# Kernel optimization log

Hardware: AMD Instinct MI355X
Metric: run time of the kernel (lower is better)

Reference implementation:

```python
import jax, jax.numpy as jnp
import numpy as np

B, C, OUTC, H, W, K, P, S = 4, 64, 64, 128, 128, 3, 1, 1
KK = K * K


def setup_inputs() -> dict:
    key = jax.random.key(0)
    ks = jax.random.split(key, 5)
    x = jax.random.normal(ks[0], (B, C, H, W), dtype=jnp.float32)
    # small-scale offset weights keep learned offsets in a realistic few-pixel range
    w_off = jax.random.normal(ks[1], (2 * KK, C, 3, 3), dtype=jnp.float32) * 0.05
    b_off = jnp.zeros((2 * KK,), dtype=jnp.float32)
    w_mask = jax.random.normal(ks[2], (KK, C, 3, 3), dtype=jnp.float32) * 0.05
    b_mask = jnp.zeros((KK,), dtype=jnp.float32)
    w_dcn = jax.random.normal(ks[3], (OUTC, C, K, K), dtype=jnp.float32) * (1.0 / np.sqrt(C * KK))
    b_dcn = jnp.zeros((OUTC,), dtype=jnp.float32)
    return {"x": x, "w_off": w_off, "b_off": b_off, "w_mask": w_mask,
            "b_mask": b_mask, "w_dcn": w_dcn, "b_dcn": b_dcn}


def _conv3x3(x, w, b):
    y = jax.lax.conv_general_dilated(x, w, (1, 1), ((1, 1), (1, 1)),
                                     dimension_numbers=("NCHW", "OIHW", "NCHW"))
    return y + b[None, :, None, None]


def _deform_conv(x, offset, mask, w, b):
    # torchvision DeformConv2d (v2, modulated). offset layout: [B, kk, (dy,dx), H, W]
    Ho = (H + 2 * P - K) // S + 1
    Wo = (W + 2 * P - K) // S + 1
    off = offset.reshape(B, KK, 2, Ho, Wo)
    dy, dx = off[:, :, 0], off[:, :, 1]                      # [B,kk,Ho,Wo]
    ki, kj = jnp.meshgrid(jnp.arange(K), jnp.arange(K), indexing="ij")
    ki = ki.reshape(KK).astype(jnp.float32)
    kj = kj.reshape(KK).astype(jnp.float32)
    hg = (jnp.arange(Ho) * S - P).astype(jnp.float32)
    wg = (jnp.arange(Wo) * S - P).astype(jnp.float32)
    py = dy + ki[None, :, None, None] + hg[None, None, :, None]   # sample y coord
    px = dx + kj[None, :, None, None] + wg[None, None, None, :]   # sample x coord

    y0f = jnp.floor(py)
    x0f = jnp.floor(px)
    ly = py - y0f
    lx = px - x0f
    y0 = y0f.astype(jnp.int32)
    x0 = x0f.astype(jnp.int32)

    x_flat = x.reshape(B, C, H * W)

    def sample(yi, xi, wgt):
        valid = (yi >= 0) & (yi < H) & (xi >= 0) & (xi < W)
        idx = jnp.clip(yi, 0, H - 1) * W + jnp.clip(xi, 0, W - 1)  # [B,kk,Ho,Wo]
        g = jax.vmap(lambda xb, ib: xb[:, ib])(x_flat, idx)        # [B,C,kk,Ho,Wo]
        return g * (wgt * valid)[:, None]

    acc = (sample(y0, x0, (1 - ly) * (1 - lx))
           + sample(y0, x0 + 1, (1 - ly) * lx)
           + sample(y0 + 1, x0, ly * (1 - lx))
           + sample(y0 + 1, x0 + 1, ly * lx))                      # [B,C,kk,Ho,Wo]
    acc = acc * mask.reshape(B, 1, KK, Ho, Wo)
    out = jnp.einsum("bckhw,ock->bohw", acc, w.reshape(OUTC, C, KK))
    return out + b[None, :, None, None]


def reference(x, w_off, b_off, w_mask, b_mask, w_dcn, b_dcn):
    offset = _conv3x3(x, w_off, b_off)
    mask = jax.nn.sigmoid(_conv3x3(x, w_mask, b_mask))
    out = _deform_conv(x, offset, mask, w_dcn, b_dcn)
    return out, offset
```

## Files before the change

### kernel.cpp

```cpp
#include <hip/hip_runtime.h>
#include <hip/hip_bf16.h>
#include <math.h>

#define BB 4
#define CC 64
#define OCN 64
#define HH 128
#define WW 128
#define HW (HH*WW)
#define KKN 9
#define CK 576
#define APAD 200

typedef short short8 __attribute__((ext_vector_type(8)));
typedef float floatx4 __attribute__((ext_vector_type(4)));
typedef unsigned int uintx4 __attribute__((ext_vector_type(4)));

__device__ __forceinline__ float bf2f(__hip_bfloat16 h) {
    unsigned short u = *reinterpret_cast<unsigned short*>(&h);
    return __uint_as_float(((unsigned)u) << 16);
}
__device__ __forceinline__ short f2bfs(float f) {
    __hip_bfloat16 h = __float2bfloat16(f);
    return *reinterpret_cast<short*>(&h);
}
__device__ __forceinline__ uintx4 as_u4(short8 v) {
    union { short8 s; uintx4 u; } x; x.s = v; return x.u;
}
__device__ __forceinline__ float blo(unsigned d) { return __uint_as_float(d << 16); }
__device__ __forceinline__ float bhi(unsigned d) { return __uint_as_float(d & 0xffff0000u); }

__global__ __launch_bounds__(256) void transpose_prep(
    const float* __restrict__ x,
    const float* __restrict__ w_dcn, const float* __restrict__ w_off,
    const float* __restrict__ b_off, const float* __restrict__ w_mask,
    const float* __restrict__ b_mask,
    __hip_bfloat16* __restrict__ xt, __hip_bfloat16* __restrict__ wTf,
    __hip_bfloat16* __restrict__ wOf, float* __restrict__ rebias)
{
    int blk = blockIdx.x;
    int tid = threadIdx.x;
    if (blk < BB * 512) {
        __shared__ float tile[64][33];
        int pixbase = (blk & 511) * 32;
        int b       = blk >> 9;
        const float* xb = x + (size_t)b * CC * HW;
        int p = tid & 31;
        #pragma unroll
        for (int i = 0; i < 8; ++i) {
            int c = (tid >> 5) * 8 + i;
            tile[c][p] = xb[(size_t)c * HW + pixbase + p];
        }
        __syncthreads();
        __hip_bfloat16* xo = xt + ((size_t)b * HW + pixbase) * CC;
        #pragma unroll
        for (int i = 0; i < 4; ++i) {
            int idx = tid + i * 256;
            int pixl = idx >> 5, c2 = idx & 31;
            unsigned short lo = (unsigned short)(unsigned)f2bfs(tile[2 * c2][pixl]);
            unsigned short hi = (unsigned short)(unsigned)f2bfs(tile[2 * c2 + 1][pixl]);
            unsigned packed = lo | ((unsigned)hi << 16);
            *reinterpret_cast<unsigned*>(&xo[(size_t)pixl * CC + c2 * 2]) = packed;
        }
        return;
    }
    int i = (blk - BB * 512) * 256 + tid;
    if (i < 18 * 4 * 64 * 8) {
        int jj = i & 7;
        int l  = (i >> 3) & 63;
        int nt = (i >> 9) & 3;
        int s  = i >> 11;
        int oc = nt * 16 + (l & 15);
        int kk = s * 32 + ((l >> 4) << 3) + jj;
        int c  = kk & 63;
        int kt = kk >> 6;
        wTf[i] = __float2bfloat16(w_dcn[(oc * CC + c) * 9 + kt]);
    }
    int j = i - 18 * 4 * 64 * 8;
    if (j >= 0 && j < 18 * 2 * 64 * 8) {
        int jj = j & 7;
        int l  = (j >> 3) & 63;
        int nt = (j >> 9) & 1;
        int s  = j >> 10;
        int oc = nt * 16 + (l & 15);
        int kk = s * 32 + ((l >> 4) << 3) + jj;
        int c  = kk & 63;
        int kt = kk >> 6;
        float v = 0.0f;
        if (oc < 18)      v = w_off[(oc * CC + c) * 9 + kt];
        else if (oc < 27) v = w_mask[((oc - 18) * CC + c) * 9 + kt];
        wOf[j] = __float2bfloat16(v);
    }
    int r = j - 18 * 2 * 64 * 8;
    if (r >= 0 && r < 27) rebias[r] = (r < 18) ? b_off[r] : b_mask[r - 18];
}

__global__ __launch_bounds__(256, 8) void offmask(
    const __hip_bfloat16* __restrict__ xt,
    const __hip_bfloat16* __restrict__ wOf, const float* __restrict__ rebias,
    float* __restrict__ off_out, float* __restrict__ mask_out)
{
    __shared__ __align__(16) __hip_bfloat16 accs[32][APAD];

    int tid  = threadIdx.x;
    int lane = tid & 63;
    int wv   = __builtin_amdgcn_readfirstlane(tid >> 6);
    int nt   = wv & 1;
    int pg   = wv >> 1;
    int c8   = tid & 7;
    int spix = (tid >> 3) & 31;

    int wo0 = (blockIdx.x & 3) * 32;
    int row = (blockIdx.x >> 2) & (HH - 1);
    int b   = blockIdx.x >> 9;

    floatx4 accv = {0, 0, 0, 0};
    const __hip_bfloat16* xtb = xt + (size_t)b * HW * CC;
    const short8 zero8 = {0,0,0,0,0,0,0,0};
    int kreg = (lane >> 4) << 3;

    for (int chunk = 0; chunk < 3; ++chunk) {
        int y = row + chunk - 1;
        bool yvalid = (unsigned)y < (unsigned)HH;
        short8 v[3];
        #pragma unroll
        for (int kl = 0; kl < 3; ++kl) {
            int xw = wo0 + spix + kl - 1;
            bool valid = yvalid && ((unsigned)xw < (unsigned)WW);
            v[kl] = zero8;
            if (valid)
                v[kl] = *reinterpret_cast<const short8*>(xtb + ((size_t)y * WW + xw) * CC + c8 * 8);
        }
        #pragma unroll
        for (int kl = 0; kl < 3; ++kl)
            *reinterpret_cast<short8*>(&accs[spix][kl * 64 + c8 * 8]) = v[kl];
        __syncthreads();

        #pragma unroll
        for (int step = 0; step < 6; ++step) {
            int s = chunk * 6 + step;
            short8 bfrag = *(reinterpret_cast<const short8*>(wOf) + (size_t)(s * 2 + nt) * 64 + lane);
            short8 a = *reinterpret_cast<const short8*>(&accs[pg * 16 + (lane & 15)][step * 32 + kreg]);
            accv = __builtin_amdgcn_mfma_f32_16x16x32_bf16(a, bfrag, accv, 0, 0, 0);
        }
        if (chunk < 2) __syncthreads();
    }

    int oc = nt * 16 + (lane & 15);
    int pcol = wo0 + pg * 16 + ((lane >> 4) << 2);
    if (oc < 18) {
        float bias = rebias[oc];
        floatx4 o = accv;
        o[0] += bias; o[1] += bias; o[2] += bias; o[3] += bias;
        *reinterpret_cast<floatx4*>(&off_out[(((size_t)b * 18 + oc) * HH + row) * WW + pcol]) = o;
    } else if (oc < 27) {
        float bias = rebias[oc];
        floatx4 o = accv;
        #pragma unroll
        for (int q = 0; q < 4; ++q) o[q] = 1.0f / (1.0f + expf(-(o[q] + bias)));
        *reinterpret_cast<floatx4*>(&mask_out[(((size_t)b * 9 + (oc - 18)) * HH + row) * WW + pcol]) = o;
    }
}

__global__ __launch_bounds__(256, 8) void deform(
    const __hip_bfloat16* __restrict__ xt,
    const float* __restrict__ off, const float* __restrict__ mask,
    const __hip_bfloat16* __restrict__ wTf, const float* __restrict__ b_dcn,
    float* __restrict__ out)
{
    __shared__ __align__(16) __hip_bfloat16 accs[32][APAD];
    __shared__ uintx4 tabs[KKN][32];

    int tid  = threadIdx.x;
    int lane = tid & 63;
    int wv   = __builtin_amdgcn_readfirstlane(tid >> 6);
    int pix  = tid >> 3;
    int c8   = tid & 7;

    int wo0 = (blockIdx.x & 3) * 32;
    int row = (blockIdx.x >> 2) & (HH - 1);
    int b   = blockIdx.x >> 9;

    for (int e = tid; e < KKN * 32; e += 256) {
        int k = e >> 5, p = e & 31;
        int wo = wo0 + p;
        float dy = off[((b * 18 + 2 * k    ) * HH + row) * WW + wo];
        float dx = off[((b * 18 + 2 * k + 1) * HH + row) * WW + wo];
        float m  = mask[((b * 9 + k) * HH + row) * WW + wo];
        float py = dy + (float)(k / 3) + (float)(row - 1);
        float px = dx + (float)(k % 3) + (float)(wo - 1);
        float y0f = floorf(py), x0f = floorf(px);
        float ly = py - y0f, lx = px - x0f;
        int y0 = (int)y0f, x0 = (int)x0f;
        uintx4 rec;
        #pragma unroll
        for (int t = 0; t < 4; ++t) {
            int yi = y0 + (t >> 1), xi = x0 + (t & 1);
            float wy = (t >> 1) ? ly : 1.0f - ly;
            float wx = (t & 1)  ? lx : 1.0f - lx;
            bool valid = ((unsigned)yi < (unsigned)HH) && ((unsigned)xi < (unsigned)WW);
            int yc = min(max(yi, 0), HH - 1);
            int xc = min(max(xi, 0), WW - 1);
            __hip_bfloat16 hw = __float2bfloat16(valid ? wy * wx * m : 0.0f);
            unsigned short wb = *reinterpret_cast<unsigned short*>(&hw);
            rec[t] = (unsigned)(yc * WW + xc) | ((unsigned)wb << 16);
        }
        tabs[k][p] = rec;
    }
    __syncthreads();

    const char* xtb = (const char*)(xt + (size_t)b * HW * CC);
    int co = c8 * 16;

    short8 buf[2][4];
    uintx4 tb[2];
    floatx4 accv[2] = {{0,0,0,0},{0,0,0,0}};
    int kreg = (lane >> 4) << 3;

#define ISSUE(G9) do { \
    uintx4 _t = tabs[(G9)][pix]; \
    tb[(G9) & 1] = _t; \
    buf[(G9) & 1][0] = *(const short8*)(xtb + ((_t[0] & 0xffffu) << 7) + co); \
    buf[(G9) & 1][1] = *(const short8*)(xtb + ((_t[1] & 0xffffu) << 7) + co); \
    buf[(G9) & 1][2] = *(const short8*)(xtb + ((_t[2] & 0xffffu) << 7) + co); \
    buf[(G9) & 1][3] = *(const short8*)(xtb + ((_t[3] & 0xffffu) << 7) + co); \
} while (0)

#define COMBINE(G9) do { \
    float aA[8] = {0,0,0,0,0,0,0,0}; \
    _Pragma("unroll") \
    for (int t = 0; t < 4; ++t) { \
        float wt = __uint_as_float(tb[(G9) & 1][t] & 0xffff0000u); \
        uintx4 dA = as_u4(buf[(G9) & 1][t]); \
        _Pragma("unroll") \
        for (int jq = 0; jq < 4; ++jq) { \
            aA[2 * jq]     = fmaf(wt, blo(dA[jq]), aA[2 * jq]); \
            aA[2 * jq + 1] = fmaf(wt, bhi(dA[jq]), aA[2 * jq + 1]); \
        } \
    } \
    short8 oA; \
    _Pragma("unroll") \
    for (int jq = 0; jq < 8; ++jq) { oA[jq] = f2bfs(aA[jq]); } \
    *reinterpret_cast<short8*>(&accs[pix][((G9) % 3) * 64 + c8 * 8]) = oA; \
} while (0)

#define MFMA_CHUNK(CH) do { \
    _Pragma("unroll") \
    for (int step = 0; step < 6; ++step) { \
        int s = (CH) * 6 + step; \
        short8 bfrag = *(reinterpret_cast<const short8*>(wTf) + (size_t)(s * 4 + wv) * 64 + lane); \
        _Pragma("unroll") \
        for (int pg = 0; pg < 2; ++pg) { \
            short8 a = *reinterpret_cast<const short8*>(&accs[pg * 16 + (lane & 15)][step * 32 + kreg]); \
            accv[pg] = __builtin_amdgcn_mfma_f32_16x16x32_bf16(a, bfrag, accv[pg], 0, 0, 0); \
        } \
    } \
} while (0)

    ISSUE(0);
    ISSUE(1); COMBINE(0);
    ISSUE(2); COMBINE(1); COMBINE(2);
    __syncthreads();
    ISSUE(3);
    MFMA_CHUNK(0);
    asm volatile("s_waitcnt lgkmcnt(0)" ::: "memory");
    __builtin_amdgcn_s_barrier();
    ISSUE(4); COMBINE(3);
    ISSUE(5); COMBINE(4); COMBINE(5);
    __syncthreads();
    ISSUE(6);
    MFMA_CHUNK(1);
    asm volatile("s_waitcnt lgkmcnt(0)" ::: "memory");
    __builtin_amdgcn_s_barrier();
    ISSUE(7); COMBINE(6);
    ISSUE(8); COMBINE(7); COMBINE(8);
    __syncthreads();
    MFMA_CHUNK(2);

#undef ISSUE
#undef COMBINE
#undef MFMA_CHUNK

    int oc = wv * 16 + (lane & 15);
    float bias = b_dcn[oc];
    #pragma unroll
    for (int pg = 0; pg < 2; ++pg) {
        int pcol = wo0 + pg * 16 + ((lane >> 4) << 2);
        floatx4 o = accv[pg];
        o[0] += bias; o[1] += bias; o[2] += bias; o[3] += bias;
        *reinterpret_cast<floatx4*>(&out[(((size_t)b * OCN + oc) * HH + row) * WW + pcol]) = o;
    }
}

extern "C" void kernel_launch(void* const* d_in, const int* in_sizes, int n_in,
                              void* d_out, int out_size, void* d_ws, size_t ws_size,
                              hipStream_t stream) {
    const float* x      = (const float*)d_in[0];
    const float* w_off  = (const float*)d_in[1];
    const float* b_off  = (const float*)d_in[2];
    const float* w_mask = (const float*)d_in[3];
    const float* b_mask = (const float*)d_in[4];
    const float* w_dcn  = (const float*)d_in[5];
    const float* b_dcn  = (const float*)d_in[6];

    float* out     = (float*)d_out;
    float* off_out = out + (size_t)BB * OCN * HW;

    float* mask_ws = (float*)d_ws;
    float* rebias  = mask_ws + (size_t)BB * 9 * HW;
    __hip_bfloat16* xt  = (__hip_bfloat16*)(rebias + 32);
    __hip_bfloat16* wTf = xt + (size_t)BB * HW * CC;
    __hip_bfloat16* wOf = wTf + 18 * 4 * 64 * 8;

    int prep_total  = 18 * 4 * 64 * 8 + 18 * 2 * 64 * 8 + 27;
    int prep_blocks = (prep_total + 255) / 256;
    transpose_prep<<<BB * 512 + prep_blocks, 256, 0, stream>>>(
        x, w_dcn, w_off, b_off, w_mask, b_mask, xt, wTf, wOf, rebias);

    offmask<<<BB * HH * 4, 256, 0, stream>>>(xt, wOf, rebias, off_out, mask_ws);

    deform<<<BB * HH * 4, 256, 0, stream>>>(xt, off_out, mask_ws, wTf, b_dcn, out);
}
```

Baseline: 44.64 us.

## Fuse offset/mask conv into deform kernel via shared-memory handoff; vectorize transpose store

Merges the offset/mask convolution kernel into the deformable-conv kernel. Each block computes its own 32-pixel row segment of offsets and sigmoid mask with MFMA, stages them in shared memory, and builds the bilinear sampling table from there. This removes a kernel launch and the global write/read round trip of the mask workspace and offsets. The transpose prep also now writes 16-byte packed bf16 vectors instead of 4-byte stores. The cost is more LDS and registers per block, which may reduce occupancy under the 256,8 launch bounds.

```diff
diff --git a/kernel.cpp b/kernel.cpp
--- a/kernel.cpp
+++ b/kernel.cpp
@@ -53,15 +53,12 @@
         }
         __syncthreads();
         __hip_bfloat16* xo = xt + ((size_t)b * HW + pixbase) * CC;
-        #pragma unroll
-        for (int i = 0; i < 4; ++i) {
-            int idx = tid + i * 256;
-            int pixl = idx >> 5, c2 = idx & 31;
-            unsigned short lo = (unsigned short)(unsigned)f2bfs(tile[2 * c2][pixl]);
-            unsigned short hi = (unsigned short)(unsigned)f2bfs(tile[2 * c2 + 1][pixl]);
-            unsigned packed = lo | ((unsigned)hi << 16);
-            *reinterpret_cast<unsigned*>(&xo[(size_t)pixl * CC + c2 * 2]) = packed;
-        }
+        int pixl = tid >> 3;
+        int c8t  = tid & 7;
+        short8 o;
+        #pragma unroll
+        for (int i = 0; i < 8; ++i) o[i] = f2bfs(tile[c8t * 8 + i][pixl]);
+        *reinterpret_cast<short8*>(&xo[(size_t)pixl * CC + c8t * 8]) = o;
         return;
     }
     int i = (blk - BB * 512) * 256 + tid;
@@ -95,30 +92,35 @@
     if (r >= 0 && r < 27) rebias[r] = (r < 18) ? b_off[r] : b_mask[r - 18];
 }
 
-__global__ __launch_bounds__(256, 8) void offmask(
+__global__ __launch_bounds__(256, 8) void deform_fused(
     const __hip_bfloat16* __restrict__ xt,
-    const __hip_bfloat16* __restrict__ wOf, const float* __restrict__ rebias,
-    float* __restrict__ off_out, float* __restrict__ mask_out)
+    const __hip_bfloat16* __restrict__ wTf, const __hip_bfloat16* __restrict__ wOf,
+    const float* __restrict__ rebias, const float* __restrict__ b_dcn,
+    float* __restrict__ off_out, float* __restrict__ out)
 {
     __shared__ __align__(16) __hip_bfloat16 accs[32][APAD];
+    __shared__ uintx4 tabs[KKN][32];
+    __shared__ float offs_l[18][33];
+    __shared__ float ms_l[KKN][33];
 
     int tid  = threadIdx.x;
     int lane = tid & 63;
     int wv   = __builtin_amdgcn_readfirstlane(tid >> 6);
+    int pix  = tid >> 3;
+    int c8   = tid & 7;
+    int spix = (tid >> 3) & 31;
     int nt   = wv & 1;
     int pg   = wv >> 1;
-    int c8   = tid & 7;
-    int spix = (tid >> 3) & 31;
 
     int wo0 = (blockIdx.x & 3) * 32;
     int row = (blockIdx.x >> 2) & (HH - 1);
     int b   = blockIdx.x >> 9;
 
-    floatx4 accv = {0, 0, 0, 0};
-    const __hip_bfloat16* xtb = xt + (size_t)b * HW * CC;
+    const __hip_bfloat16* xtb16 = xt + (size_t)b * HW * CC;
     const short8 zero8 = {0,0,0,0,0,0,0,0};
     int kreg = (lane >> 4) << 3;
 
+    floatx4 accom = {0, 0, 0, 0};
     for (int chunk = 0; chunk < 3; ++chunk) {
         int y = row + chunk - 1;
         bool yvalid = (unsigned)y < (unsigned)HH;
@@ -129,7 +131,7 @@
             bool valid = yvalid && ((unsigned)xw < (unsigned)WW);
             v[kl] = zero8;
             if (valid)
-                v[kl] = *reinterpret_cast<const short8*>(xtb + ((size_t)y * WW + xw) * CC + c8 * 8);
+                v[kl] = *reinterpret_cast<const short8*>(xtb16 + ((size_t)y * WW + xw) * CC + c8 * 8);
         }
         #pragma unroll
         for (int kl = 0; kl < 3; ++kl)
@@ -141,54 +143,39 @@
             int s = chunk * 6 + step;
             short8 bfrag = *(reinterpret_cast<const short8*>(wOf) + (size_t)(s * 2 + nt) * 64 + lane);
             short8 a = *reinterpret_cast<const short8*>(&accs[pg * 16 + (lane & 15)][step * 32 + kreg]);
-            accv = __builtin_amdgcn_mfma_f32_16x16x32_bf16(a, bfrag, accv, 0, 0, 0);
-        }
-        if (chunk < 2) __syncthreads();
-    }
-
-    int oc = nt * 16 + (lane & 15);
-    int pcol = wo0 + pg * 16 + ((lane >> 4) << 2);
-    if (oc < 18) {
-        float bias = rebias[oc];
-        floatx4 o = accv;
-        o[0] += bias; o[1] += bias; o[2] += bias; o[3] += bias;
-        *reinterpret_cast<floatx4*>(&off_out[(((size_t)b * 18 + oc) * HH + row) * WW + pcol]) = o;
-    } else if (oc < 27) {
-        float bias = rebias[oc];
-        floatx4 o = accv;
-        #pragma unroll
-        for (int q = 0; q < 4; ++q) o[q] = 1.0f / (1.0f + expf(-(o[q] + bias)));
-        *reinterpret_cast<floatx4*>(&mask_out[(((size_t)b * 9 + (oc - 18)) * HH + row) * WW + pcol]) = o;
-    }
-}
-
-__global__ __launch_bounds__(256, 8) void deform(
-    const __hip_bfloat16* __restrict__ xt,
-    const float* __restrict__ off, const float* __restrict__ mask,
-    const __hip_bfloat16* __restrict__ wTf, const float* __restrict__ b_dcn,
-    float* __restrict__ out)
-{
-    __shared__ __align__(16) __hip_bfloat16 accs[32][APAD];
-    __shared__ uintx4 tabs[KKN][32];
-
-    int tid  = threadIdx.x;
-    int lane = tid & 63;
-    int wv   = __builtin_amdgcn_readfirstlane(tid >> 6);
-    int pix  = tid >> 3;
-    int c8   = tid & 7;
-
-    int wo0 = (blockIdx.x & 3) * 32;
-    int row = (blockIdx.x >> 2) & (HH - 1);
-    int b   = blockIdx.x >> 9;
+            accom = __builtin_amdgcn_mfma_f32_16x16x32_bf16(a, bfrag, accom, 0, 0, 0);
+        }
+        __syncthreads();
+    }
+
+    {
+        int oc = nt * 16 + (lane & 15);
+        int pcol = pg * 16 + ((lane >> 4) << 2);
+        if (oc < 18) {
+            float bias = rebias[oc];
+            floatx4 o = accom;
+            o[0] += bias; o[1] += bias; o[2] += bias; o[3] += bias;
+            *reinterpret_cast<floatx4*>(&off_out[(((size_t)b * 18 + oc) * HH + row) * WW + wo0 + pcol]) = o;
+            offs_l[oc][pcol]     = o[0];
+            offs_l[oc][pcol + 1] = o[1];
+            offs_l[oc][pcol + 2] = o[2];
+            offs_l[oc][pcol + 3] = o[3];
+        } else if (oc < 27) {
+            float bias = rebias[oc];
+            #pragma unroll
+            for (int q = 0; q < 4; ++q)
+                ms_l[oc - 18][pcol + q] = 1.0f / (1.0f + expf(-(accom[q] + bias)));
+        }
+    }
+    __syncthreads();
 
     for (int e = tid; e < KKN * 32; e += 256) {
         int k = e >> 5, p = e & 31;
-        int wo = wo0 + p;
-        float dy = off[((b * 18 + 2 * k    ) * HH + row) * WW + wo];
-        float dx = off[((b * 18 + 2 * k + 1) * HH + row) * WW + wo];
-        float m  = mask[((b * 9 + k) * HH + row) * WW + wo];
+        float dy = offs_l[2 * k][p];
+        float dx = offs_l[2 * k + 1][p];
+        float m  = ms_l[k][p];
         float py = dy + (float)(k / 3) + (float)(row - 1);
-        float px = dx + (float)(k % 3) + (float)(wo - 1);
+        float px = dx + (float)(k % 3) + (float)(wo0 + p - 1);
         float y0f = floorf(py), x0f = floorf(px);
         float ly = py - y0f, lx = px - x0f;
         int y0 = (int)y0f, x0 = (int)x0f;
@@ -209,13 +196,12 @@
     }
     __syncthreads();
 
-    const char* xtb = (const char*)(xt + (size_t)b * HW * CC);
+    const char* xtb = (const char*)xtb16;
     int co = c8 * 16;
 
     short8 buf[2][4];
     uintx4 tb[2];
     floatx4 accv[2] = {{0,0,0,0},{0,0,0,0}};
-    int kreg = (lane >> 4) << 3;
 
 #define ISSUE(G9) do { \
     uintx4 _t = tabs[(G9)][pix]; \
@@ -250,9 +236,9 @@
         int s = (CH) * 6 + step; \
         short8 bfrag = *(reinterpret_cast<const short8*>(wTf) + (size_t)(s * 4 + wv) * 64 + lane); \
         _Pragma("unroll") \
-        for (int pg = 0; pg < 2; ++pg) { \
-            short8 a = *reinterpret_cast<const short8*>(&accs[pg * 16 + (lane & 15)][step * 32 + kreg]); \
-            accv[pg] = __builtin_amdgcn_mfma_f32_16x16x32_bf16(a, bfrag, accv[pg], 0, 0, 0); \
+        for (int pgq = 0; pgq < 2; ++pgq) { \
+            short8 a = *reinterpret_cast<const short8*>(&accs[pgq * 16 + (lane & 15)][step * 32 + kreg]); \
+            accv[pgq] = __builtin_amdgcn_mfma_f32_16x16x32_bf16(a, bfrag, accv[pgq], 0, 0, 0); \
         } \
     } \
 } while (0)
@@ -284,9 +270,9 @@
     int oc = wv * 16 + (lane & 15);
     float bias = b_dcn[oc];
     #pragma unroll
-    for (int pg = 0; pg < 2; ++pg) {
-        int pcol = wo0 + pg * 16 + ((lane >> 4) << 2);
-        floatx4 o = accv[pg];
+    for (int pgq = 0; pgq < 2; ++pgq) {
+        int pcol = wo0 + pgq * 16 + ((lane >> 4) << 2);
+        floatx4 o = accv[pgq];
         o[0] += bias; o[1] += bias; o[2] += bias; o[3] += bias;
         *reinterpret_cast<floatx4*>(&out[(((size_t)b * OCN + oc) * HH + row) * WW + pcol]) = o;
     }
@@ -306,8 +292,7 @@
     float* out     = (float*)d_out;
     float* off_out = out + (size_t)BB * OCN * HW;
 
-    float* mask_ws = (float*)d_ws;
-    float* rebias  = mask_ws + (size_t)BB * 9 * HW;
+    float* rebias  = (float*)d_ws;
     __hip_bfloat16* xt  = (__hip_bfloat16*)(rebias + 32);
     __hip_bfloat16* wTf = xt + (size_t)BB * HW * CC;
     __hip_bfloat16* wOf = wTf + 18 * 4 * 64 * 8;
@@ -317,7 +302,6 @@
     transpose_prep<<<BB * 512 + prep_blocks, 256, 0, stream>>>(
         x, w_dcn, w_off, b_off, w_mask, b_mask, xt, wTf, wOf, rebias);
 
-    offmask<<<BB * HH * 4, 256, 0, stream>>>(xt, wOf, rebias, off_out, mask_ws);
-
-    deform<<<BB * HH * 4, 256, 0, stream>>>(xt, off_out, mask_ws, wTf, b_dcn, out);
-}
+    deform_fused<<<BB * HH * 4, 256, 0, stream>>>(
+        xt, wTf, wOf, rebias, b_dcn, off_out, out);
+}
```

Measured after the change: 41.61 us. 1.07x faster.
